# Kernel tuning notes

Measured on AMD Instinct MI355X. Metric: run time of the kernel, lower is better.

## Reference

```python
import jax, jax.numpy as jnp
import numpy as np

B, T, C, H = 4, 2048, 768, 12
D = C // H  # head dim = 64
EPS = 1e-5


def setup_inputs() -> dict:
    key = jax.random.key(0)
    ks = jax.random.split(key, 12)
    s = lambda fan_in: 1.0 / np.sqrt(fan_in)
    return {
        "x": jax.random.normal(ks[0], (B, T, C), dtype=jnp.float32),
        "ln1_g": jnp.ones((C,), jnp.float32),
        "ln1_b": jnp.zeros((C,), jnp.float32),
        "w_attn": jax.random.normal(ks[1], (C, 3 * C), jnp.float32) * s(C),
        "b_attn": jnp.zeros((3 * C,), jnp.float32),
        "w_aproj": jax.random.normal(ks[2], (C, C), jnp.float32) * s(C),
        "b_aproj": jnp.zeros((C,), jnp.float32),
        "ln2_g": jnp.ones((C,), jnp.float32),
        "ln2_b": jnp.zeros((C,), jnp.float32),
        "w_fc": jax.random.normal(ks[3], (C, 4 * C), jnp.float32) * s(C),
        "b_fc": jnp.zeros((4 * C,), jnp.float32),
        "w_mproj": jax.random.normal(ks[4], (4 * C, C), jnp.float32) * s(4 * C),
        "b_mproj": jnp.zeros((C,), jnp.float32),
    }


def _layernorm(x, g, b):
    mu = jnp.mean(x, axis=-1, keepdims=True)
    var = jnp.mean(jnp.square(x - mu), axis=-1, keepdims=True)
    return (x - mu) * jax.lax.rsqrt(var + EPS) * g + b


def _attention(h, w_attn, b_attn, w_aproj, b_aproj):
    qkv = h @ w_attn + b_attn                          # [B,T,3C]
    q, k, v = jnp.split(qkv, 3, axis=-1)
    q = q.reshape(B, T, H, D)
    k = k.reshape(B, T, H, D)
    v = v.reshape(B, T, H, D)
    att = jnp.einsum("bqhd,bkhd->bhqk", q, k) * (1.0 / np.sqrt(D))
    causal = jnp.tril(jnp.ones((T, T), bool))
    att = jnp.where(causal, att, -jnp.inf)
    att = jax.nn.softmax(att, axis=-1)
    y = jnp.einsum("bhqk,bkhd->bqhd", att, v).reshape(B, T, C)
    return y @ w_aproj + b_aproj


def reference(x, ln1_g, ln1_b, w_attn, b_attn, w_aproj, b_aproj,
              ln2_g, ln2_b, w_fc, b_fc, w_mproj, b_mproj):
    x = x + _attention(_layernorm(x, ln1_g, ln1_b), w_attn, b_attn, w_aproj, b_aproj)
    h = _layernorm(x, ln2_g, ln2_b)
    h = jax.nn.gelu(h @ w_fc + b_fc, approximate=True)  # tanh approximation, matches F.gelu(approximate='tanh')
    x = x + (h @ w_mproj + b_mproj)
    return x
```

## Files before the change

kernel.cpp:

```cpp
#include <hip/hip_runtime.h>


typedef unsigned short ushortT;
typedef unsigned int uintT;
typedef __attribute__((ext_vector_type(8))) __bf16 bf16x8;
typedef __attribute__((ext_vector_type(4))) float f32x4;

#define MFMA16(a, b, c) __builtin_amdgcn_mfma_f32_16x16x32_bf16(a, b, c, 0, 0, 0)

__device__ inline float b2f(ushortT u) {
  return __uint_as_float(((uintT)u) << 16);
}
__device__ inline ushortT f2b(float f) {
  uintT x = __float_as_uint(f);
  uintT r = x + 0x7fffu + ((x >> 16) & 1u);
  return (ushortT)(r >> 16);
}
__device__ inline uintT pack_bf2(float a, float b) {
  return __builtin_amdgcn_perm(__float_as_uint(b), __float_as_uint(a),
                               0x07060302u);
}

__device__ inline float fast_exp2(float x) {
#if __has_builtin(__builtin_amdgcn_exp2f)
  return __builtin_amdgcn_exp2f(x);
#else
  return exp2f(x);
#endif
}

__device__ inline float gelu_tanh(float v) {
  float t = 0.7978845608028654f * (v + 0.044715f * v * v * v);
  return v / (1.0f + __expf(-2.0f * t));
}

__device__ __forceinline__ void glds16(const ushortT* g, ushortT* l) {
  __builtin_amdgcn_global_load_lds(
      (const __attribute__((address_space(1))) unsigned int*)(const void*)g,
      (__attribute__((address_space(3))) unsigned int*)(void*)l, 16, 0, 0);
}

__global__ __launch_bounds__(256) void detect_dtype(
    const ushortT* __restrict__ w, int* __restrict__ flag) {
  __shared__ int red;
  if (threadIdx.x == 0) red = 0;
  __syncthreads();
  int crazy = 0;
  for (int i = threadIdx.x; i < 4096; i += 256) {
    uintT e = (w[2 * i] >> 7) & 0xFF;
    if (e >= 150) crazy = 1;
  }
  if (crazy) atomicOr(&red, 1);
  __syncthreads();
  if (threadIdx.x == 0) *flag = red;
}

struct VecArgs {
  const void* src[8];
  int n[8];
  int dstoff[8];
};
__global__ __launch_bounds__(256) void convert_vecs(
    VecArgs a, ushortT* __restrict__ pv, const int* __restrict__ flag) {
  int fl = *flag;
  int t = blockIdx.y;
  int i = blockIdx.x * 256 + threadIdx.x;
  if (i >= a.n[t]) return;
  float v = fl ? ((const float*)a.src[t])[i] : b2f(((const ushortT*)a.src[t])[i]);
  pv[a.dstoff[t] + i] = f2b(v);
}

__global__ __launch_bounds__(256) void transpose_any(
    const void* __restrict__ in, ushortT* __restrict__ out, int K, int N,
    const int* __restrict__ flag) {
  __shared__ ushortT t[32][33];
  int fl = *flag;
  int n0 = blockIdx.x * 32, k0 = blockIdx.y * 32;
  int x = threadIdx.x, y0 = threadIdx.y;
#pragma unroll
  for (int i = y0; i < 32; i += 8) {
    size_t idx = (size_t)(k0 + i) * N + n0 + x;
    t[i][x] = fl ? f2b(((const float*)in)[idx]) : ((const ushortT*)in)[idx];
  }
  __syncthreads();
#pragma unroll
  for (int i = y0; i < 32; i += 8)
    out[(size_t)(n0 + i) * K + k0 + x] = t[x][i];
}

__global__ __launch_bounds__(256) void vtrans_kernel(
    const ushortT* __restrict__ qkv, ushortT* __restrict__ vt) {
  const int T = 2048, C3 = 2304;
  __shared__ ushortT tile[64][65];
  int bh = blockIdx.y;
  int b = bh / 12, h = bh % 12;
  int t0 = blockIdx.x * 64;
  int col = threadIdx.x & 63, rowi = threadIdx.x >> 6;
#pragma unroll
  for (int rr = rowi; rr < 64; rr += 4)
    tile[rr][col] =
        qkv[((size_t)(b * T + t0 + rr)) * C3 + 1536 + h * 64 + col];
  __syncthreads();
#pragma unroll
  for (int dd = rowi; dd < 64; dd += 4)
    vt[((size_t)bh * 64 + dd) * T + t0 + col] = tile[col][dd];
}

template <int MODE>
__global__ __launch_bounds__(256) void ln_kernel(
    const void* __restrict__ xin, const ushortT* __restrict__ g,
    const ushortT* __restrict__ bb, ushortT* __restrict__ out,
    const int* __restrict__ flag) {
  const int C = 768;
  bool f32;
  if constexpr (MODE == 1) f32 = true; else f32 = (*flag != 0);
  size_t base = (size_t)blockIdx.x * C;
  int tid = threadIdx.x;
  const float* xf = (const float*)xin;
  const ushortT* xb = (const ushortT*)xin;
  float v0 = f32 ? xf[base + tid]       : b2f(xb[base + tid]);
  float v1 = f32 ? xf[base + tid + 256] : b2f(xb[base + tid + 256]);
  float v2 = f32 ? xf[base + tid + 512] : b2f(xb[base + tid + 512]);
  float s = v0 + v1 + v2;
  float q = v0 * v0 + v1 * v1 + v2 * v2;
#pragma unroll
  for (int off = 32; off; off >>= 1) {
    s += __shfl_xor(s, off);
    q += __shfl_xor(q, off);
  }
  __shared__ float as_[4], aq_[4];
  if ((tid & 63) == 0) { as_[tid >> 6] = s; aq_[tid >> 6] = q; }
  __syncthreads();
  s = as_[0] + as_[1] + as_[2] + as_[3];
  q = aq_[0] + aq_[1] + aq_[2] + aq_[3];
  float mu = s * (1.0f / 768.0f);
  float var = q * (1.0f / 768.0f) - mu * mu;
  float rs = rsqrtf(var + 1e-5f);
  ushortT* orow = out + base;
  orow[tid]       = f2b((v0 - mu) * rs * b2f(g[tid])       + b2f(bb[tid]));
  orow[tid + 256] = f2b((v1 - mu) * rs * b2f(g[tid + 256]) + b2f(bb[tid + 256]));
  orow[tid + 512] = f2b((v2 - mu) * rs * b2f(g[tid + 512]) + b2f(bb[tid + 512]));
}

template <int EPI, int BN>
__global__ __launch_bounds__(256, 2) void gemm_8p(
    const ushortT* __restrict__ A, const ushortT* __restrict__ Bt,
    const ushortT* __restrict__ bias, const void* __restrict__ res,
    void* __restrict__ out, int N, int K, int nbm, int nbn,
    const int* __restrict__ flag) {
  constexpr int MI = (BN == 256) ? 8 : 4;
  constexpr int NI = 4;
  constexpr int LOADS = 2 + BN / 64;
  __shared__ ushortT As3[3][128 * 32];
  __shared__ ushortT Bs3[3][BN * 32];
  int fl = (EPI >= 2) ? *flag : 0;
  int tid = threadIdx.x;
  int lane = tid & 63, wave = tid >> 6;
  int quad = lane >> 4, n = lane & 15;
  int wm, wn;
  if constexpr (BN == 256) { wm = 0; wn = wave * 64; }
  else { wm = (wave >> 1) * 64; wn = (wave & 1) * 64; }
  int l = blockIdx.x;
  int xcd = l & 7, j = l >> 3;
  int m0 = (xcd * (nbm >> 3) + j / nbn) * 128;
  int n0 = (j % nbn) * BN;

  int trow = tid >> 2;
  int tc = (((tid & 3) ^ ((trow >> 1) & 3)) << 3);
  const ushortT* ga = A + (size_t)(m0 + trow) * K + tc;
  const ushortT* gb = Bt + (size_t)(n0 + trow) * K + tc;

  const int cs = (quad ^ ((n >> 1) & 3)) << 3;

  int kt = K >> 5;
  f32x4 acc[MI][NI] = {};

  auto stage = [&](int tt, int slot) {
    int k0 = tt << 5;
    ushortT* la = &As3[slot][0] + wave * 512;
    ushortT* lb = &Bs3[slot][0] + wave * 512;
    glds16(ga + k0, la);
    glds16(ga + (size_t)64 * K + k0, la + 2048);
    glds16(gb + k0, lb);
    glds16(gb + (size_t)64 * K + k0, lb + 2048);
    if constexpr (BN == 256) {
      glds16(gb + (size_t)128 * K + k0, lb + 4096);
      glds16(gb + (size_t)192 * K + k0, lb + 6144);
    }
  };

  stage(0, 0);
  stage(1, 1);
  if constexpr (BN == 256)
    asm volatile("s_waitcnt vmcnt(6)" ::: "memory");
  else
    asm volatile("s_waitcnt vmcnt(4)" ::: "memory");
  __builtin_amdgcn_s_barrier();

  int cur = 0;
  for (int t = 0; t < kt; ++t) {
    const ushortT* ca = &As3[cur][0];
    const ushortT* cb = &Bs3[cur][0];
    int nxt = cur + 2; if (nxt >= 3) nxt -= 3;
    bool pf = (t + 2) < kt;
    int pk0 = (t + 2) << 5;
    ushortT* la = &As3[nxt][0] + wave * 512;
    ushortT* lb = &Bs3[nxt][0] + wave * 512;

    bf16x8 af[4], bfr[NI];
#pragma unroll
    for (int i = 0; i < 4; ++i)
      af[i] = *(const bf16x8*)(ca + (wm + i * 16 + n) * 32 + cs);
#pragma unroll
    for (int i = 0; i < NI; ++i)
      bfr[i] = *(const bf16x8*)(cb + (wn + i * 16 + n) * 32 + cs);
    if (pf) {
      glds16(ga + pk0, la);
      glds16(ga + (size_t)64 * K + pk0, la + 2048);
      glds16(gb + pk0, lb);
      if constexpr (BN == 128) glds16(gb + (size_t)64 * K + pk0, lb + 2048);
    }
    __builtin_amdgcn_s_barrier();
    __builtin_amdgcn_s_setprio(1);
#pragma unroll
    for (int mi = 0; mi < 4; ++mi)
#pragma unroll
      for (int ni = 0; ni < NI; ++ni)
        acc[mi][ni] = MFMA16(af[mi], bfr[ni], acc[mi][ni]);
    __builtin_amdgcn_s_setprio(0);
    if constexpr (BN == 256) {
      __builtin_amdgcn_s_barrier();
#pragma unroll
      for (int i = 0; i < 4; ++i)
        af[i] = *(const bf16x8*)(ca + (64 + i * 16 + n) * 32 + cs);
      if (pf) {
        glds16(gb + (size_t)64 * K + pk0, lb + 2048);
        glds16(gb + (size_t)128 * K + pk0, lb + 4096);
        glds16(gb + (size_t)192 * K + pk0, lb + 6144);
      }
      __builtin_amdgcn_s_barrier();
      __builtin_amdgcn_s_setprio(1);
#pragma unroll
      for (int mi = 0; mi < 4; ++mi)
#pragma unroll
        for (int ni = 0; ni < NI; ++ni)
          acc[4 + mi][ni] = MFMA16(af[mi], bfr[ni], acc[4 + mi][ni]);
      __builtin_amdgcn_s_setprio(0);
    }
    if (pf) {
      if constexpr (BN == 256)
        asm volatile("s_waitcnt vmcnt(6)" ::: "memory");
      else
        asm volatile("s_waitcnt vmcnt(4)" ::: "memory");
    } else {
      asm volatile("s_waitcnt vmcnt(0)" ::: "memory");
    }
    __builtin_amdgcn_s_barrier();

    cur = cur + 1; if (cur == 3) cur = 0;
  }

#pragma unroll
  for (int mi = 0; mi < MI; ++mi) {
#pragma unroll
    for (int ni = 0; ni < NI; ++ni) {
      int gc = n0 + wn + ni * 16 + n;
      float bv = b2f(bias[gc]);
      int gr0 = m0 + wm + mi * 16 + quad * 4;
#pragma unroll
      for (int r = 0; r < 4; ++r) {
        size_t idx = (size_t)(gr0 + r) * N + gc;
        float v = acc[mi][ni][r] + bv;
        if constexpr (EPI == 1) v = gelu_tanh(v);
        if constexpr (EPI == 2) {
          v += fl ? ((const float*)res)[idx] : b2f(((const ushortT*)res)[idx]);
          ((float*)out)[idx] = v;
        } else if constexpr (EPI == 3) {
          v += ((const float*)res)[idx];
          if (fl) ((float*)out)[idx] = v;
          else    ((ushortT*)out)[idx] = f2b(v);
        } else {
          ((ushortT*)out)[idx] = f2b(v);
        }
      }
    }
  }
}

__global__ __launch_bounds__(256) void attn_kernel(
    const ushortT* __restrict__ qkv, const ushortT* __restrict__ vt,
    ushortT* __restrict__ y) {
  const int T = 2048, C3 = 2304;
  constexpr int LDP = 72;
  __shared__ ushortT Ks[2][64 * 64];
  __shared__ ushortT Vs[2][64 * 64];
  __shared__ ushortT Ps[4 * 16 * LDP];
  int bh = blockIdx.y;
  int b = bh / 12, h = bh % 12;
  int pj = blockIdx.x;
  int tid = threadIdx.x;
  int lane = tid & 63, wave = tid >> 6;
  int quad = lane >> 4, n = lane & 15, n7 = n & 7;

  const ushortT* base = qkv + (size_t)b * T * C3;
  const ushortT* kbase = base + 768 + h * 64;
  const ushortT* vbase = vt + (size_t)bh * 64 * T;
  ushortT* myP = Ps + wave * 16 * LDP;

  const float QS = 0.18033688011112042f;
  const float MB = 20.0f;

  int qtA = pj, qtB = 31 - pj;
  int nA = qtA + 1, ntot = 33;

  int srow = lane >> 3, scol = lane & 7;
  const ushortT* kg =
      kbase + (size_t)(wave * 16 + srow) * C3 + ((scol ^ srow) << 3);
  const ushortT* vg =
      vbase + (size_t)(wave * 16 + srow) * T + ((scol ^ srow) << 3);

  const int c0 = (quad ^ n7) << 3;
  const int c1 = ((4 + quad) ^ n7) << 3;

  int qt = qtA;
  int qw = qt * 64 + wave * 16;
  bf16x8 aq[2];
  {
    const ushortT* qrow = base + (size_t)(qw + n) * C3 + h * 64 + quad * 8;
#pragma unroll
    for (int dh = 0; dh < 2; ++dh) {
      union { ushortT u[8]; bf16x8 v; } tmp;
#pragma unroll
      for (int j = 0; j < 8; ++j) tmp.u[j] = f2b(b2f(qrow[dh * 32 + j]) * QS);
      aq[dh] = tmp.v;
    }
  }
  f32x4 Ot[4] = {};
  float l_ = 0.f;

  auto stage = [&](int kt_, int buf) {
    int kof = kt_ << 6;
    ushortT* lk = &Ks[buf][0] + wave * 1024;
    ushortT* lv = &Vs[buf][0] + wave * 1024;
    glds16(kg + (size_t)kof * C3, lk);
    glds16(kg + (size_t)(kof + 8) * C3, lk + 512);
    glds16(vg + kof, lv);
    glds16(vg + (size_t)8 * T + kof, lv + 512);
  };

  stage(0, 0);
  __syncthreads();

  int cur = 0;
  for (int t = 0; t < ntot; ++t) {
    int kt = (t < nA) ? t : t - nA;
    if (t + 1 < ntot) {
      int ktn = (t + 1 < nA) ? t + 1 : t + 1 - nA;
      stage(ktn, cur ^ 1);
    }
    const ushortT* ks = &Ks[cur][0];
    const ushortT* vs = &Vs[cur][0];

    f32x4 St[4];
#pragma unroll
    for (int g = 0; g < 4; ++g) {
      bf16x8 ka0 = *(const bf16x8*)(ks + (g * 16 + n) * 64 + c0);
      bf16x8 ka1 = *(const bf16x8*)(ks + (g * 16 + n) * 64 + c1);
      f32x4 z = {};
      z = MFMA16(ka0, aq[0], z);
      St[g] = MFMA16(ka1, aq[1], z);
    }
    if (kt == qt) {
      int lim = wave * 16 + n;
#pragma unroll
      for (int g = 0; g < 4; ++g)
#pragma unroll
        for (int r = 0; r < 4; ++r)
          if (g * 16 + quad * 4 + r > lim) St[g][r] = -1e30f;
    }
    float ls = 0.f;
#pragma unroll
    for (int g = 0; g < 4; ++g) {
      float p0 = fast_exp2(St[g][0] - MB);
      float p1 = fast_exp2(St[g][1] - MB);
      float p2 = fast_exp2(St[g][2] - MB);
      float p3 = fast_exp2(St[g][3] - MB);
      ls += (p0 + p1) + (p2 + p3);
      uint2 pk;
      pk.x = pack_bf2(p0, p1);
      pk.y = pack_bf2(p2, p3);
      *(uint2*)(myP + n * LDP + g * 16 + quad * 4) = pk;
    }
    ls += __shfl_xor(ls, 16);
    ls += __shfl_xor(ls, 32);
    l_ += ls;

    bf16x8 pb0 = *(const bf16x8*)(myP + n * LDP + quad * 8);
    bf16x8 pb1 = *(const bf16x8*)(myP + n * LDP + 32 + quad * 8);
#pragma unroll
    for (int dt = 0; dt < 4; ++dt) {
      bf16x8 va0 = *(const bf16x8*)(vs + (dt * 16 + n) * 64 + c0);
      bf16x8 va1 = *(const bf16x8*)(vs + (dt * 16 + n) * 64 + c1);
      Ot[dt] = MFMA16(va0, pb0, Ot[dt]);
      Ot[dt] = MFMA16(va1, pb1, Ot[dt]);
    }

    if (kt == qt) {
      float inv = 1.0f / l_;
      int qg = qw + n;
#pragma unroll
      for (int dt = 0; dt < 4; ++dt) {
        uint2 o;
        o.x = pack_bf2(Ot[dt][0] * inv, Ot[dt][1] * inv);
        o.y = pack_bf2(Ot[dt][2] * inv, Ot[dt][3] * inv);
        *(uint2*)(y + (size_t)(b * T + qg) * 768 + h * 64 + dt * 16 +
                  quad * 4) = o;
      }
      if (t + 1 < ntot) {
        qt = qtB;
        qw = qt * 64 + wave * 16;
        const ushortT* qrow =
            base + (size_t)(qw + n) * C3 + h * 64 + quad * 8;
#pragma unroll
        for (int dh = 0; dh < 2; ++dh) {
          union { ushortT u[8]; bf16x8 v; } tmp;
#pragma unroll
          for (int j = 0; j < 8; ++j)
            tmp.u[j] = f2b(b2f(qrow[dh * 32 + j]) * QS);
          aq[dh] = tmp.v;
        }
#pragma unroll
        for (int dt = 0; dt < 4; ++dt)
#pragma unroll
          for (int r = 0; r < 4; ++r) Ot[dt][r] = 0.f;
        l_ = 0.f;
      }
    }
    __syncthreads();
    cur ^= 1;
  }
}

extern "C" void kernel_launch(void* const* d_in, const int* in_sizes, int n_in,
                              void* d_out, int out_size, void* d_ws,
                              size_t ws_size, hipStream_t stream) {
  (void)in_sizes; (void)n_in; (void)out_size; (void)ws_size;
  const void* x       = d_in[0];
  const void* w_attn  = d_in[3];
  const void* w_aproj = d_in[5];
  const void* w_fc    = d_in[9];
  const void* w_mproj = d_in[11];

  char* ws = (char*)d_ws;
  ushortT* h1  = (ushortT*)(ws);
  ushortT* qkv = (ushortT*)(ws + 12582912);
  ushortT* yb  = (ushortT*)(ws + 50331648);
  float*   x1  = (float*)(ws + 62914560);
  ushortT* fcg = (ushortT*)(ws + 88080384);
  ushortT* wT0 = (ushortT*)(ws + 138412032);
  ushortT* wT1 = (ushortT*)(ws + 141950976);
  ushortT* wT2 = (ushortT*)(ws + 143130624);
  ushortT* wT3 = (ushortT*)(ws + 147849216);
  ushortT* pv  = (ushortT*)(ws + 152567808);
  int*     flag = (int*)(ws + 152600576);
  ushortT* vt  = h1;
  ushortT* h2  = yb;

  const int O_LN1G = 0, O_LN1B = 768, O_BATT = 1536, O_BAPR = 3840,
            O_LN2G = 4608, O_LN2B = 5376, O_BFC = 6144, O_BMPR = 9216;

  detect_dtype<<<1, 256, 0, stream>>>((const ushortT*)w_fc, flag);

  VecArgs va;
  va.src[0] = d_in[1];  va.n[0] = 768;  va.dstoff[0] = O_LN1G;
  va.src[1] = d_in[2];  va.n[1] = 768;  va.dstoff[1] = O_LN1B;
  va.src[2] = d_in[4];  va.n[2] = 2304; va.dstoff[2] = O_BATT;
  va.src[3] = d_in[6];  va.n[3] = 768;  va.dstoff[3] = O_BAPR;
  va.src[4] = d_in[7];  va.n[4] = 768;  va.dstoff[4] = O_LN2G;
  va.src[5] = d_in[8];  va.n[5] = 768;  va.dstoff[5] = O_LN2B;
  va.src[6] = d_in[10]; va.n[6] = 3072; va.dstoff[6] = O_BFC;
  va.src[7] = d_in[12]; va.n[7] = 768;  va.dstoff[7] = O_BMPR;
  convert_vecs<<<dim3(12, 8), 256, 0, stream>>>(va, pv, flag);

  dim3 tb(32, 8);
  transpose_any<<<dim3(72, 24), tb, 0, stream>>>(w_attn, wT0, 768, 2304, flag);
  transpose_any<<<dim3(24, 24), tb, 0, stream>>>(w_aproj, wT1, 768, 768, flag);
  transpose_any<<<dim3(96, 24), tb, 0, stream>>>(w_fc, wT2, 768, 3072, flag);
  transpose_any<<<dim3(24, 96), tb, 0, stream>>>(w_mproj, wT3, 3072, 768, flag);

  ln_kernel<0><<<8192, 256, 0, stream>>>(x, pv + O_LN1G, pv + O_LN1B, h1, flag);
  gemm_8p<0, 256><<<576, 256, 0, stream>>>(
      h1, wT0, pv + O_BATT, nullptr, qkv, 2304, 768, 64, 9, flag);
  vtrans_kernel<<<dim3(32, 48), 256, 0, stream>>>(qkv, vt);
  attn_kernel<<<dim3(16, 48), 256, 0, stream>>>(qkv, vt, yb);
  gemm_8p<2, 128><<<384, 256, 0, stream>>>(
      yb, wT1, pv + O_BAPR, x, x1, 768, 768, 64, 6, flag);
  ln_kernel<1><<<8192, 256, 0, stream>>>(x1, pv + O_LN2G, pv + O_LN2B, h2, flag);
  gemm_8p<1, 256><<<768, 256, 0, stream>>>(
      h2, wT2, pv + O_BFC, nullptr, fcg, 3072, 768, 64, 12, flag);
  gemm_8p<3, 128><<<384, 256, 0, stream>>>(
      fcg, wT3, pv + O_BMPR, x1, d_out, 768, 3072, 64, 6, flag);
}
```

Baseline: 419.1 us.

## Switch GEMMs to 256x256 tiles with 8 waves and split-K mproj

Replaces the 128xBN, 4-wave GEMM with a 256x256-tile, 512-thread kernel that splits the B-tile loads across two half-steps. The goal is higher arithmetic intensity and less global traffic per FLOP. The MLP projection (K=3072) becomes a two-way split-K that writes fp32 partials, and a new reduce kernel adds the partials, residual and bias. The aproj GEMM now launches only 96 blocks, which may underfill the GPU, and the larger tiles raise LDS and register pressure.

```diff
diff --git a/kernel.cpp b/kernel.cpp
--- a/kernel.cpp
+++ b/kernel.cpp
@@ -142,59 +142,50 @@
   orow[tid + 512] = f2b((v2 - mu) * rs * b2f(g[tid + 512]) + b2f(bb[tid + 512]));
 }
 
-template <int EPI, int BN>
-__global__ __launch_bounds__(256, 2) void gemm_8p(
+template <int EPI>
+__global__ __launch_bounds__(512, 2) void gemm256(
     const ushortT* __restrict__ A, const ushortT* __restrict__ Bt,
     const ushortT* __restrict__ bias, const void* __restrict__ res,
-    void* __restrict__ out, int N, int K, int nbm, int nbn,
+    void* __restrict__ out, int N, int K, int lda, int ldb, int nbn,
     const int* __restrict__ flag) {
-  constexpr int MI = (BN == 256) ? 8 : 4;
-  constexpr int NI = 4;
-  constexpr int LOADS = 2 + BN / 64;
-  __shared__ ushortT As3[3][128 * 32];
-  __shared__ ushortT Bs3[3][BN * 32];
-  int fl = (EPI >= 2) ? *flag : 0;
+  __shared__ ushortT As3[3][256 * 32];
+  __shared__ ushortT Bs3[3][256 * 32];
+  int fl = (EPI == 2) ? *flag : 0;
   int tid = threadIdx.x;
   int lane = tid & 63, wave = tid >> 6;
   int quad = lane >> 4, n = lane & 15;
-  int wm, wn;
-  if constexpr (BN == 256) { wm = 0; wn = wave * 64; }
-  else { wm = (wave >> 1) * 64; wn = (wave & 1) * 64; }
+  int wm = (wave >> 2) * 128, wn = (wave & 3) * 64;
   int l = blockIdx.x;
   int xcd = l & 7, j = l >> 3;
-  int m0 = (xcd * (nbm >> 3) + j / nbn) * 128;
-  int n0 = (j % nbn) * BN;
+  int per = 4 * nbn;
+  int js = j % per, sp = j / per;
+  int m0 = (xcd * 4 + js / nbn) * 256;
+  int n0 = (js % nbn) * 256;
+  int koff = sp * K;
 
   int trow = tid >> 2;
-  int tc = (((tid & 3) ^ ((trow >> 1) & 3)) << 3);
-  const ushortT* ga = A + (size_t)(m0 + trow) * K + tc;
-  const ushortT* gb = Bt + (size_t)(n0 + trow) * K + tc;
+  int tc = (((tid & 3) ^ ((tid >> 3) & 3)) << 3);
+  const ushortT* ga = A + (size_t)(m0 + trow) * lda + koff + tc;
+  const ushortT* gb = Bt + (size_t)(n0 + trow) * ldb + koff + tc;
 
   const int cs = (quad ^ ((n >> 1) & 3)) << 3;
 
   int kt = K >> 5;
-  f32x4 acc[MI][NI] = {};
+  f32x4 acc[8][4] = {};
 
   auto stage = [&](int tt, int slot) {
     int k0 = tt << 5;
     ushortT* la = &As3[slot][0] + wave * 512;
     ushortT* lb = &Bs3[slot][0] + wave * 512;
     glds16(ga + k0, la);
-    glds16(ga + (size_t)64 * K + k0, la + 2048);
+    glds16(ga + (size_t)128 * lda + k0, la + 4096);
     glds16(gb + k0, lb);
-    glds16(gb + (size_t)64 * K + k0, lb + 2048);
-    if constexpr (BN == 256) {
-      glds16(gb + (size_t)128 * K + k0, lb + 4096);
-      glds16(gb + (size_t)192 * K + k0, lb + 6144);
-    }
+    glds16(gb + (size_t)128 * ldb + k0, lb + 4096);
   };
 
   stage(0, 0);
   stage(1, 1);
-  if constexpr (BN == 256)
-    asm volatile("s_waitcnt vmcnt(6)" ::: "memory");
-  else
-    asm volatile("s_waitcnt vmcnt(4)" ::: "memory");
+  asm volatile("s_waitcnt vmcnt(4)" ::: "memory");
   __builtin_amdgcn_s_barrier();
 
   int cur = 0;
@@ -207,83 +198,108 @@
     ushortT* la = &As3[nxt][0] + wave * 512;
     ushortT* lb = &Bs3[nxt][0] + wave * 512;
 
-    bf16x8 af[4], bfr[NI];
+    bf16x8 af[4], bfr[4];
 #pragma unroll
     for (int i = 0; i < 4; ++i)
       af[i] = *(const bf16x8*)(ca + (wm + i * 16 + n) * 32 + cs);
 #pragma unroll
-    for (int i = 0; i < NI; ++i)
+    for (int i = 0; i < 4; ++i)
       bfr[i] = *(const bf16x8*)(cb + (wn + i * 16 + n) * 32 + cs);
     if (pf) {
       glds16(ga + pk0, la);
-      glds16(ga + (size_t)64 * K + pk0, la + 2048);
-      glds16(gb + pk0, lb);
-      if constexpr (BN == 128) glds16(gb + (size_t)64 * K + pk0, lb + 2048);
+      glds16(ga + (size_t)128 * lda + pk0, la + 4096);
     }
     __builtin_amdgcn_s_barrier();
     __builtin_amdgcn_s_setprio(1);
 #pragma unroll
     for (int mi = 0; mi < 4; ++mi)
 #pragma unroll
-      for (int ni = 0; ni < NI; ++ni)
+      for (int ni = 0; ni < 4; ++ni)
         acc[mi][ni] = MFMA16(af[mi], bfr[ni], acc[mi][ni]);
     __builtin_amdgcn_s_setprio(0);
-    if constexpr (BN == 256) {
-      __builtin_amdgcn_s_barrier();
-#pragma unroll
-      for (int i = 0; i < 4; ++i)
-        af[i] = *(const bf16x8*)(ca + (64 + i * 16 + n) * 32 + cs);
-      if (pf) {
-        glds16(gb + (size_t)64 * K + pk0, lb + 2048);
-        glds16(gb + (size_t)128 * K + pk0, lb + 4096);
-        glds16(gb + (size_t)192 * K + pk0, lb + 6144);
-      }
-      __builtin_amdgcn_s_barrier();
-      __builtin_amdgcn_s_setprio(1);
-#pragma unroll
-      for (int mi = 0; mi < 4; ++mi)
-#pragma unroll
-        for (int ni = 0; ni < NI; ++ni)
-          acc[4 + mi][ni] = MFMA16(af[mi], bfr[ni], acc[4 + mi][ni]);
-      __builtin_amdgcn_s_setprio(0);
-    }
+    __builtin_amdgcn_s_barrier();
+
+    bf16x8 af2[4];
+#pragma unroll
+    for (int i = 0; i < 4; ++i)
+      af2[i] = *(const bf16x8*)(ca + (wm + 64 + i * 16 + n) * 32 + cs);
     if (pf) {
-      if constexpr (BN == 256)
-        asm volatile("s_waitcnt vmcnt(6)" ::: "memory");
-      else
-        asm volatile("s_waitcnt vmcnt(4)" ::: "memory");
-    } else {
-      asm volatile("s_waitcnt vmcnt(0)" ::: "memory");
+      glds16(gb + pk0, lb);
+      glds16(gb + (size_t)128 * ldb + pk0, lb + 4096);
     }
     __builtin_amdgcn_s_barrier();
+    __builtin_amdgcn_s_setprio(1);
+#pragma unroll
+    for (int mi = 0; mi < 4; ++mi)
+#pragma unroll
+      for (int ni = 0; ni < 4; ++ni)
+        acc[4 + mi][ni] = MFMA16(af2[mi], bfr[ni], acc[4 + mi][ni]);
+    __builtin_amdgcn_s_setprio(0);
+    if (pf) asm volatile("s_waitcnt vmcnt(4)" ::: "memory");
+    else    asm volatile("s_waitcnt vmcnt(0)" ::: "memory");
+    __builtin_amdgcn_s_barrier();
 
     cur = cur + 1; if (cur == 3) cur = 0;
   }
 
-#pragma unroll
-  for (int mi = 0; mi < MI; ++mi) {
-#pragma unroll
-    for (int ni = 0; ni < NI; ++ni) {
+  float* po = nullptr;
+  if constexpr (EPI == 4) po = sp ? (float*)res : (float*)out;
+#pragma unroll
+  for (int mi = 0; mi < 8; ++mi) {
+#pragma unroll
+    for (int ni = 0; ni < 4; ++ni) {
       int gc = n0 + wn + ni * 16 + n;
-      float bv = b2f(bias[gc]);
+      float bv = (EPI == 4) ? 0.0f : b2f(bias[gc]);
       int gr0 = m0 + wm + mi * 16 + quad * 4;
 #pragma unroll
       for (int r = 0; r < 4; ++r) {
         size_t idx = (size_t)(gr0 + r) * N + gc;
         float v = acc[mi][ni][r] + bv;
-        if constexpr (EPI == 1) v = gelu_tanh(v);
-        if constexpr (EPI == 2) {
+        if constexpr (EPI == 1) {
+          v = gelu_tanh(v);
+          ((ushortT*)out)[idx] = f2b(v);
+        } else if constexpr (EPI == 2) {
           v += fl ? ((const float*)res)[idx] : b2f(((const ushortT*)res)[idx]);
           ((float*)out)[idx] = v;
-        } else if constexpr (EPI == 3) {
-          v += ((const float*)res)[idx];
-          if (fl) ((float*)out)[idx] = v;
-          else    ((ushortT*)out)[idx] = f2b(v);
+        } else if constexpr (EPI == 4) {
+          po[idx] = v;
         } else {
           ((ushortT*)out)[idx] = f2b(v);
         }
       }
     }
+  }
+}
+
+__global__ __launch_bounds__(256) void mproj_reduce(
+    const float* __restrict__ P0, const float* __restrict__ P1,
+    const float* __restrict__ res, const ushortT* __restrict__ bias,
+    void* __restrict__ out, const int* __restrict__ flag) {
+  int fl = *flag;
+  size_t i0 = ((size_t)blockIdx.x * 256 + threadIdx.x) * 8;
+  int col = (int)(i0 % 768);
+  float o[8];
+#pragma unroll
+  for (int j = 0; j < 8; j += 4) {
+    float4 a = *(const float4*)(P0 + i0 + j);
+    float4 b = *(const float4*)(P1 + i0 + j);
+    float4 r = *(const float4*)(res + i0 + j);
+    o[j + 0] = a.x + b.x + r.x + b2f(bias[col + j + 0]);
+    o[j + 1] = a.y + b.y + r.y + b2f(bias[col + j + 1]);
+    o[j + 2] = a.z + b.z + r.z + b2f(bias[col + j + 2]);
+    o[j + 3] = a.w + b.w + r.w + b2f(bias[col + j + 3]);
+  }
+  if (fl) {
+    float* of = (float*)out;
+#pragma unroll
+    for (int j = 0; j < 8; ++j) of[i0 + j] = o[j];
+  } else {
+    uint4 pk;
+    pk.x = pack_bf2(o[0], o[1]);
+    pk.y = pack_bf2(o[2], o[3]);
+    pk.z = pack_bf2(o[4], o[5]);
+    pk.w = pack_bf2(o[6], o[7]);
+    *(uint4*)((ushortT*)out + i0) = pk;
   }
 }
 
@@ -465,6 +481,8 @@
   int*     flag = (int*)(ws + 152600576);
   ushortT* vt  = h1;
   ushortT* h2  = yb;
+  float*   P0  = (float*)(ws);
+  float*   P1  = (float*)(ws + 25165824);
 
   const int O_LN1G = 0, O_LN1B = 768, O_BATT = 1536, O_BAPR = 3840,
             O_LN2G = 4608, O_LN2B = 5376, O_BFC = 6144, O_BMPR = 9216;
@@ -489,15 +507,17 @@
   transpose_any<<<dim3(24, 96), tb, 0, stream>>>(w_mproj, wT3, 3072, 768, flag);
 
   ln_kernel<0><<<8192, 256, 0, stream>>>(x, pv + O_LN1G, pv + O_LN1B, h1, flag);
-  gemm_8p<0, 256><<<576, 256, 0, stream>>>(
-      h1, wT0, pv + O_BATT, nullptr, qkv, 2304, 768, 64, 9, flag);
+  gemm256<0><<<288, 512, 0, stream>>>(
+      h1, wT0, pv + O_BATT, nullptr, qkv, 2304, 768, 768, 768, 9, flag);
   vtrans_kernel<<<dim3(32, 48), 256, 0, stream>>>(qkv, vt);
   attn_kernel<<<dim3(16, 48), 256, 0, stream>>>(qkv, vt, yb);
-  gemm_8p<2, 128><<<384, 256, 0, stream>>>(
-      yb, wT1, pv + O_BAPR, x, x1, 768, 768, 64, 6, flag);
+  gemm256<2><<<96, 512, 0, stream>>>(
+      yb, wT1, pv + O_BAPR, x, x1, 768, 768, 768, 768, 3, flag);
   ln_kernel<1><<<8192, 256, 0, stream>>>(x1, pv + O_LN2G, pv + O_LN2B, h2, flag);
-  gemm_8p<1, 256><<<768, 256, 0, stream>>>(
-      h2, wT2, pv + O_BFC, nullptr, fcg, 3072, 768, 64, 12, flag);
-  gemm_8p<3, 128><<<384, 256, 0, stream>>>(
-      fcg, wT3, pv + O_BMPR, x1, d_out, 768, 3072, 64, 6, flag);
-}
+  gemm256<1><<<384, 512, 0, stream>>>(
+      h2, wT2, pv + O_BFC, nullptr, fcg, 3072, 768, 768, 768, 12, flag);
+  gemm256<4><<<192, 512, 0, stream>>>(
+      fcg, wT3, nullptr, P1, P0, 768, 1536, 3072, 3072, 3, flag);
+  mproj_reduce<<<3072, 256, 0, stream>>>(
+      P0, P1, x1, pv + O_BMPR, d_out, flag);
+}
```

New measurement: 468.2 us. 1.12x slower.

## Split-K the MLP projection GEMM into two halves with a reduction kernel

Applied to the files above, without the earlier changes.

The final 3072-deep projection GEMM now runs as a split-K launch with twice the blocks, each covering half of K and writing fp32 partials to two workspace buffers. A new elementwise kernel sums the partials, adds bias and residual, and writes the output in the detected dtype. The aim is better occupancy of the GPU's compute units, since the original launch of 384 blocks underfilled it. The cost is an extra kernel launch plus about 50 MB of fp32 partial-buffer writes and reads.

```diff
diff --git a/kernel.cpp b/kernel.cpp
--- a/kernel.cpp
+++ b/kernel.cpp
@@ -146,14 +146,13 @@
 __global__ __launch_bounds__(256, 2) void gemm_8p(
     const ushortT* __restrict__ A, const ushortT* __restrict__ Bt,
     const ushortT* __restrict__ bias, const void* __restrict__ res,
-    void* __restrict__ out, int N, int K, int nbm, int nbn,
+    void* __restrict__ out, int N, int K, int lda, int nbm, int nbn,
     const int* __restrict__ flag) {
   constexpr int MI = (BN == 256) ? 8 : 4;
   constexpr int NI = 4;
-  constexpr int LOADS = 2 + BN / 64;
   __shared__ ushortT As3[3][128 * 32];
   __shared__ ushortT Bs3[3][BN * 32];
-  int fl = (EPI >= 2) ? *flag : 0;
+  int fl = (EPI == 2) ? *flag : 0;
   int tid = threadIdx.x;
   int lane = tid & 63, wave = tid >> 6;
   int quad = lane >> 4, n = lane & 15;
@@ -162,13 +161,16 @@
   else { wm = (wave >> 1) * 64; wn = (wave & 1) * 64; }
   int l = blockIdx.x;
   int xcd = l & 7, j = l >> 3;
-  int m0 = (xcd * (nbm >> 3) + j / nbn) * 128;
-  int n0 = (j % nbn) * BN;
+  int per = (nbm >> 3) * nbn;
+  int js = j % per, sp = j / per;
+  int m0 = (xcd * (nbm >> 3) + js / nbn) * 128;
+  int n0 = (js % nbn) * BN;
+  int koff = sp * K;
 
   int trow = tid >> 2;
   int tc = (((tid & 3) ^ ((trow >> 1) & 3)) << 3);
-  const ushortT* ga = A + (size_t)(m0 + trow) * K + tc;
-  const ushortT* gb = Bt + (size_t)(n0 + trow) * K + tc;
+  const ushortT* ga = A + (size_t)(m0 + trow) * lda + koff + tc;
+  const ushortT* gb = Bt + (size_t)(n0 + trow) * lda + koff + tc;
 
   const int cs = (quad ^ ((n >> 1) & 3)) << 3;
 
@@ -180,12 +182,12 @@
     ushortT* la = &As3[slot][0] + wave * 512;
     ushortT* lb = &Bs3[slot][0] + wave * 512;
     glds16(ga + k0, la);
-    glds16(ga + (size_t)64 * K + k0, la + 2048);
+    glds16(ga + (size_t)64 * lda + k0, la + 2048);
     glds16(gb + k0, lb);
-    glds16(gb + (size_t)64 * K + k0, lb + 2048);
+    glds16(gb + (size_t)64 * lda + k0, lb + 2048);
     if constexpr (BN == 256) {
-      glds16(gb + (size_t)128 * K + k0, lb + 4096);
-      glds16(gb + (size_t)192 * K + k0, lb + 6144);
+      glds16(gb + (size_t)128 * lda + k0, lb + 4096);
+      glds16(gb + (size_t)192 * lda + k0, lb + 6144);
     }
   };
 
@@ -216,9 +218,10 @@
       bfr[i] = *(const bf16x8*)(cb + (wn + i * 16 + n) * 32 + cs);
     if (pf) {
       glds16(ga + pk0, la);
-      glds16(ga + (size_t)64 * K + pk0, la + 2048);
+      glds16(ga + (size_t)64 * lda + pk0, la + 2048);
       glds16(gb + pk0, lb);
-      if constexpr (BN == 128) glds16(gb + (size_t)64 * K + pk0, lb + 2048);
+      if constexpr (BN == 128)
+        glds16(gb + (size_t)64 * lda + pk0, lb + 2048);
     }
     __builtin_amdgcn_s_barrier();
     __builtin_amdgcn_s_setprio(1);
@@ -234,9 +237,9 @@
       for (int i = 0; i < 4; ++i)
         af[i] = *(const bf16x8*)(ca + (64 + i * 16 + n) * 32 + cs);
       if (pf) {
-        glds16(gb + (size_t)64 * K + pk0, lb + 2048);
-        glds16(gb + (size_t)128 * K + pk0, lb + 4096);
-        glds16(gb + (size_t)192 * K + pk0, lb + 6144);
+        glds16(gb + (size_t)64 * lda + pk0, lb + 2048);
+        glds16(gb + (size_t)128 * lda + pk0, lb + 4096);
+        glds16(gb + (size_t)192 * lda + pk0, lb + 6144);
       }
       __builtin_amdgcn_s_barrier();
       __builtin_amdgcn_s_setprio(1);
@@ -260,30 +263,68 @@
     cur = cur + 1; if (cur == 3) cur = 0;
   }
 
+  float* po = nullptr;
+  if constexpr (EPI == 4) po = sp ? (float*)res : (float*)out;
 #pragma unroll
   for (int mi = 0; mi < MI; ++mi) {
 #pragma unroll
     for (int ni = 0; ni < NI; ++ni) {
       int gc = n0 + wn + ni * 16 + n;
-      float bv = b2f(bias[gc]);
+      float bv = (EPI == 4) ? 0.0f : b2f(bias[gc]);
       int gr0 = m0 + wm + mi * 16 + quad * 4;
 #pragma unroll
       for (int r = 0; r < 4; ++r) {
         size_t idx = (size_t)(gr0 + r) * N + gc;
         float v = acc[mi][ni][r] + bv;
-        if constexpr (EPI == 1) v = gelu_tanh(v);
-        if constexpr (EPI == 2) {
+        if constexpr (EPI == 1) {
+          v = gelu_tanh(v);
+          ((ushortT*)out)[idx] = f2b(v);
+        } else if constexpr (EPI == 2) {
           v += fl ? ((const float*)res)[idx] : b2f(((const ushortT*)res)[idx]);
           ((float*)out)[idx] = v;
         } else if constexpr (EPI == 3) {
           v += ((const float*)res)[idx];
           if (fl) ((float*)out)[idx] = v;
           else    ((ushortT*)out)[idx] = f2b(v);
+        } else if constexpr (EPI == 4) {
+          po[idx] = v;
         } else {
           ((ushortT*)out)[idx] = f2b(v);
         }
       }
     }
+  }
+}
+
+__global__ __launch_bounds__(256) void mproj_reduce(
+    const float* __restrict__ P0, const float* __restrict__ P1,
+    const float* __restrict__ res, const ushortT* __restrict__ bias,
+    void* __restrict__ out, const int* __restrict__ flag) {
+  int fl = *flag;
+  size_t i0 = ((size_t)blockIdx.x * 256 + threadIdx.x) * 8;
+  int col = (int)(i0 % 768);
+  float o[8];
+#pragma unroll
+  for (int j = 0; j < 8; j += 4) {
+    float4 a = *(const float4*)(P0 + i0 + j);
+    float4 b = *(const float4*)(P1 + i0 + j);
+    float4 r = *(const float4*)(res + i0 + j);
+    o[j + 0] = a.x + b.x + r.x + b2f(bias[col + j + 0]);
+    o[j + 1] = a.y + b.y + r.y + b2f(bias[col + j + 1]);
+    o[j + 2] = a.z + b.z + r.z + b2f(bias[col + j + 2]);
+    o[j + 3] = a.w + b.w + r.w + b2f(bias[col + j + 3]);
+  }
+  if (fl) {
+    float* of = (float*)out;
+#pragma unroll
+    for (int j = 0; j < 8; ++j) of[i0 + j] = o[j];
+  } else {
+    uint4 pk;
+    pk.x = pack_bf2(o[0], o[1]);
+    pk.y = pack_bf2(o[2], o[3]);
+    pk.z = pack_bf2(o[4], o[5]);
+    pk.w = pack_bf2(o[6], o[7]);
+    *(uint4*)((ushortT*)out + i0) = pk;
   }
 }
 
@@ -465,6 +506,8 @@
   int*     flag = (int*)(ws + 152600576);
   ushortT* vt  = h1;
   ushortT* h2  = yb;
+  float*   P0  = (float*)(ws);
+  float*   P1  = (float*)(ws + 25165824);
 
   const int O_LN1G = 0, O_LN1B = 768, O_BATT = 1536, O_BAPR = 3840,
             O_LN2G = 4608, O_LN2B = 5376, O_BFC = 6144, O_BMPR = 9216;
@@ -490,14 +533,16 @@
 
   ln_kernel<0><<<8192, 256, 0, stream>>>(x, pv + O_LN1G, pv + O_LN1B, h1, flag);
   gemm_8p<0, 256><<<576, 256, 0, stream>>>(
-      h1, wT0, pv + O_BATT, nullptr, qkv, 2304, 768, 64, 9, flag);
+      h1, wT0, pv + O_BATT, nullptr, qkv, 2304, 768, 768, 64, 9, flag);
   vtrans_kernel<<<dim3(32, 48), 256, 0, stream>>>(qkv, vt);
   attn_kernel<<<dim3(16, 48), 256, 0, stream>>>(qkv, vt, yb);
   gemm_8p<2, 128><<<384, 256, 0, stream>>>(
-      yb, wT1, pv + O_BAPR, x, x1, 768, 768, 64, 6, flag);
+      yb, wT1, pv + O_BAPR, x, x1, 768, 768, 768, 64, 6, flag);
   ln_kernel<1><<<8192, 256, 0, stream>>>(x1, pv + O_LN2G, pv + O_LN2B, h2, flag);
   gemm_8p<1, 256><<<768, 256, 0, stream>>>(
-      h2, wT2, pv + O_BFC, nullptr, fcg, 3072, 768, 64, 12, flag);
-  gemm_8p<3, 128><<<384, 256, 0, stream>>>(
-      fcg, wT3, pv + O_BMPR, x1, d_out, 768, 3072, 64, 6, flag);
-}
+      h2, wT2, pv + O_BFC, nullptr, fcg, 3072, 768, 768, 64, 12, flag);
+  gemm_8p<4, 128><<<768, 256, 0, stream>>>(
+      fcg, wT3, nullptr, P1, P0, 768, 1536, 3072, 64, 6, flag);
+  mproj_reduce<<<3072, 256, 0, stream>>>(
+      P0, P1, x1, pv + O_BMPR, d_out, flag);
+}
```

Result: no change. 419.7 us (+0.2%).
